# Optimization experiments

Measured on AMD Instinct MI355X. Metric: run time of the kernel, lower is better.

The kernel has to match this reference:

```python
import jax, jax.numpy as jnp
import numpy as np

N_NODES = 20000
N_EDGES = 320000


def gcn_conv(x, W, b, src, dst, n_nodes):
    """PyG GCNConv: add self-loops, symmetric D^-1/2 (A+I) D^-1/2 normalization,
    linear transform then normalized scatter-add aggregation, plus bias."""
    x = x @ W  # [N, out]
    loop = jnp.arange(n_nodes, dtype=src.dtype)
    s = jnp.concatenate([src, loop])  # [E+N]
    d = jnp.concatenate([dst, loop])
    # degree of destination nodes (edge weight = 1), including self-loops
    deg = jax.ops.segment_sum(jnp.ones_like(d, dtype=x.dtype), d, num_segments=n_nodes)
    dinv = jnp.where(deg > 0, jax.lax.rsqrt(deg), 0.0)
    norm = dinv[s] * dinv[d]  # [E+N]
    msg = x[s] * norm[:, None]  # gather + scale, [E+N, out]
    out = jax.ops.segment_sum(msg, d, num_segments=n_nodes)  # scatter-add
    return out + b


def setup_inputs() -> dict:
    key = jax.random.key(0)
    ks = jax.random.split(key, 8)
    x = jax.random.normal(ks[0], (N_NODES, 10), dtype=jnp.float32)
    edge_index = jax.random.randint(ks[1], (2, N_EDGES), 0, N_NODES, dtype=jnp.int32)
    # Glorot-ish init for weights, zero bias (as in PyG defaults)
    def glorot(k, shape):
        lim = float(np.sqrt(6.0 / (shape[0] + shape[1])))
        return jax.random.uniform(k, shape, jnp.float32, -lim, lim)
    return {
        "x": x,
        "edge_index": edge_index,
        "W1": glorot(ks[2], (10, 256)),
        "b1": jnp.zeros((256,), jnp.float32),
        "W2": glorot(ks[3], (256, 128)),
        "b2": jnp.zeros((128,), jnp.float32),
        "W3": glorot(ks[4], (128, 1)),
        "b3": jnp.zeros((1,), jnp.float32),
    }


def reference(x, edge_index, W1, b1, W2, b2, W3, b3):
    src, dst = edge_index[0], edge_index[1]
    n = x.shape[0]
    h = jax.nn.relu(gcn_conv(x, W1, b1, src, dst, n))
    h = jax.nn.relu(gcn_conv(h, W2, b2, src, dst, n))
    out = gcn_conv(h, W3, b3, src, dst, n)
    return out.squeeze(-1)  # [N]
```

## Files before the change

kernel.cpp:

```cpp
#include <hip/hip_runtime.h>
#include <hip/hip_fp16.h>


constexpr int NN  = 20000;
constexpr int NE  = 320000;
constexpr int F0  = 10;
constexpr int F1  = 256;
constexpr int F2  = 128;
constexpr int MB  = 16;
constexpr int CAP = 64;
constexpr int EMAX = 48;

typedef _Float16 f16x8 __attribute__((ext_vector_type(8)));
typedef float    f32x4 __attribute__((ext_vector_type(4)));

constexpr int H1S = 264;
constexpr int BKC = 64;
constexpr int W2S = 72;


__global__ void k_fill(const int* __restrict__ src, const int* __restrict__ dst,
                       int* cursor, int* __restrict__ col) {
  const int t = blockIdx.x * 256 + threadIdx.x;
  if (t * 2 >= NE) return;
  const int2 s2 = *(const int2*)&src[t * 2];
  const int2 d2 = *(const int2*)&dst[t * 2];
  const int p0 = atomicAdd(&cursor[d2.x], 1) & (CAP - 1);
  col[d2.x * CAP + p0] = s2.x;
  const int p1 = atomicAdd(&cursor[d2.y], 1) & (CAP - 1);
  col[d2.y * CAP + p1] = s2.y;
}


__global__ __launch_bounds__(256) void k_prep(const float* __restrict__ W2,
                                              _Float16* __restrict__ W2t,
                                              int* __restrict__ cursor) {
  const int t = blockIdx.x * 256 + threadIdx.x;
  const int n = t >> 8;
  const int k = t & 255;
  W2t[n * 256 + k] = (_Float16)W2[k * F2 + n];
  if (t < NN) cursor[t] = 0;
}


__global__ __launch_bounds__(256) void k_gemm12(
    const float* __restrict__ x, const int* __restrict__ cursor,
    const int* __restrict__ col, const float* __restrict__ W1,
    const float* __restrict__ b1, const _Float16* __restrict__ W2t,
    _Float16* __restrict__ t2h) {
  __shared__ float alds[MB * F0];
  __shared__ float din[MB];
  __shared__ __align__(16) _Float16 h1h[MB * H1S];
  __shared__ __align__(16) _Float16 w2t[F2 * W2S];
  __shared__ unsigned short es[MB][EMAX];
  const int tid = threadIdx.x;
  const int n0 = blockIdx.x * MB;
  const uint4* W2t4 = (const uint4*)W2t;
  const int gb = ((tid >> 3) << 5) + (tid & 7);
  uint4 pf0 = W2t4[gb];
  uint4 pf1 = W2t4[gb + 1024];
  uint4 pf2 = W2t4[gb + 2048];
  uint4 pf3 = W2t4[gb + 3072];
  {
    const int m = tid >> 4;
    const int j0 = tid & 15;
    const int n = n0 + m;
    const int degraw = cursor[n];
    const int deg = min(degraw, EMAX);
    const int base = n * CAP;
    if (j0 == 0) din[m] = rsqrtf((float)(degraw + 1));
    for (int j = j0; j < deg; j += 16)
      es[m][j] = (unsigned short)col[base + j];
  }
  __syncthreads();
  {
    const int m = tid >> 4;
    const int f = tid & 15;
    if (f < F0) {
      const int n = n0 + m;
      const int deg = min(cursor[n], EMAX);
      const float di = din[m];
      float acc = x[n * F0 + f] * di;
      int j = 0;
      for (; j + 3 < deg; j += 4) {
        const int s0 = es[m][j],     s1 = es[m][j + 1];
        const int s2 = es[m][j + 2], s3 = es[m][j + 3];
        const float q0 = rsqrtf((float)(cursor[s0] + 1));
        const float q1 = rsqrtf((float)(cursor[s1] + 1));
        const float q2 = rsqrtf((float)(cursor[s2] + 1));
        const float q3 = rsqrtf((float)(cursor[s3] + 1));
        acc += x[s0 * F0 + f] * q0 + x[s1 * F0 + f] * q1 +
               x[s2 * F0 + f] * q2 + x[s3 * F0 + f] * q3;
      }
      for (; j < deg; ++j) {
        const int s = es[m][j];
        acc += x[s * F0 + f] * rsqrtf((float)(cursor[s] + 1));
      }
      alds[m * F0 + f] = di * acc;
    }
  }
  __syncthreads();
  {
    const int c = tid;
    float w1r[F0];
#pragma unroll
    for (int k = 0; k < F0; ++k) w1r[k] = W1[k * F1 + c];
    const float bb = b1[c];
#pragma unroll
    for (int m = 0; m < MB; ++m) {
      float acc = bb;
#pragma unroll
      for (int k = 0; k < F0; ++k) acc += alds[m * F0 + k] * w1r[k];
      h1h[m * H1S + c] = (_Float16)fmaxf(acc, 0.f);
    }
  }
  const int lane = tid & 63;
  const int wv   = tid >> 6;
  const int lr   = lane & 15;
  const int lg   = lane >> 4;
  const int nt0  = wv * 32;
  f32x4 acc0 = {0.f, 0.f, 0.f, 0.f};
  f32x4 acc1 = {0.f, 0.f, 0.f, 0.f};
  uint4* w2t4 = (uint4*)w2t;
  const int sb = (tid >> 3) * 9 + (tid & 7);
  for (int kc = 0; kc < F1 / BKC; ++kc) {
    __syncthreads();
    w2t4[sb]       = pf0;
    w2t4[sb + 288] = pf1;
    w2t4[sb + 576] = pf2;
    w2t4[sb + 864] = pf3;
    __syncthreads();
    if (kc + 1 < F1 / BKC) {
      const uint4* gnext = W2t4 + (kc + 1) * 8;
      pf0 = gnext[gb];
      pf1 = gnext[gb + 1024];
      pf2 = gnext[gb + 2048];
      pf3 = gnext[gb + 3072];
    }
#pragma unroll
    for (int ks = 0; ks < 2; ++ks) {
      const int kb = kc * BKC + ks * 32;
      const f16x8 av = *(const f16x8*)&h1h[lr * H1S + kb + lg * 8];
      const f16x8 b0 = *(const f16x8*)&w2t[(nt0 + lr) * W2S + ks * 32 + lg * 8];
      const f16x8 b1v = *(const f16x8*)&w2t[(nt0 + 16 + lr) * W2S + ks * 32 + lg * 8];
      acc0 = __builtin_amdgcn_mfma_f32_16x16x32_f16(av, b0, acc0, 0, 0, 0);
      acc1 = __builtin_amdgcn_mfma_f32_16x16x32_f16(av, b1v, acc1, 0, 0, 0);
    }
  }
#pragma unroll
  for (int r = 0; r < 4; ++r) {
    const int row = lg * 4 + r;
    const float dn = din[row];
    t2h[(size_t)(n0 + row) * F2 + nt0 + lr]      = (_Float16)(acc0[r] * dn);
    t2h[(size_t)(n0 + row) * F2 + nt0 + 16 + lr] = (_Float16)(acc1[r] * dn);
  }
}


__device__ inline void acc_h4(uint2 u, float& a0, float& a1, float& a2, float& a3) {
  union { uint2 u; __half2 h[2]; } pk;
  pk.u = u;
  const float2 f0 = __half22float2(pk.h[0]);
  const float2 f1 = __half22float2(pk.h[1]);
  a0 += f0.x; a1 += f0.y; a2 += f1.x; a3 += f1.y;
}

__global__ __launch_bounds__(256) void k_agg2(
    const __half* __restrict__ t2h, const int* __restrict__ cursor,
    const int* __restrict__ col, const float* __restrict__ b2,
    const float* __restrict__ W3, float* __restrict__ t3s) {
  const int wave = (blockIdx.x * 256 + threadIdx.x) >> 6;
  const int lane = threadIdx.x & 63;
  const int half = lane >> 5;
  const int li   = lane & 31;
  const int n    = wave * 2 + half;
  if (n >= NN) return;
  const int deg = cursor[n];
  const int base = n * CAP;
  const int fx = li * 4;
  float a0 = 0.f, a1 = 0.f, a2 = 0.f, a3 = 0.f;
  acc_h4(*(const uint2*)&t2h[(size_t)n * F2 + fx], a0, a1, a2, a3);
  int k = 0;
  for (; k + 15 < deg; k += 16) {
    int ss[16];
#pragma unroll
    for (int j = 0; j < 16; ++j) ss[j] = col[base + k + j];
    uint2 vv[16];
#pragma unroll
    for (int j = 0; j < 16; ++j)
      vv[j] = *(const uint2*)&t2h[(size_t)ss[j] * F2 + fx];
#pragma unroll
    for (int j = 0; j < 16; ++j) acc_h4(vv[j], a0, a1, a2, a3);
  }
  for (; k + 7 < deg; k += 8) {
    int ss[8];
#pragma unroll
    for (int j = 0; j < 8; ++j) ss[j] = col[base + k + j];
    uint2 vv[8];
#pragma unroll
    for (int j = 0; j < 8; ++j)
      vv[j] = *(const uint2*)&t2h[(size_t)ss[j] * F2 + fx];
#pragma unroll
    for (int j = 0; j < 8; ++j) acc_h4(vv[j], a0, a1, a2, a3);
  }
  for (; k + 3 < deg; k += 4) {
    int ss[4];
#pragma unroll
    for (int j = 0; j < 4; ++j) ss[j] = col[base + k + j];
    uint2 vv[4];
#pragma unroll
    for (int j = 0; j < 4; ++j)
      vv[j] = *(const uint2*)&t2h[(size_t)ss[j] * F2 + fx];
#pragma unroll
    for (int j = 0; j < 4; ++j) acc_h4(vv[j], a0, a1, a2, a3);
  }
  for (; k < deg; ++k) {
    acc_h4(*(const uint2*)&t2h[(size_t)col[base + k] * F2 + fx], a0, a1, a2, a3);
  }
  const float di = rsqrtf((float)(deg + 1));
  const float4 bb = *(const float4*)&b2[fx];
  const float4 w3 = *(const float4*)&W3[fx];
  const float h0 = fmaxf(di * a0 + bb.x, 0.f);
  const float h1 = fmaxf(di * a1 + bb.y, 0.f);
  const float h2 = fmaxf(di * a2 + bb.z, 0.f);
  const float h3 = fmaxf(di * a3 + bb.w, 0.f);
  float p = (h0 * w3.x + h1 * w3.y) + (h2 * w3.z + h3 * w3.w);
#pragma unroll
  for (int off = 16; off > 0; off >>= 1) p += __shfl_down(p, off);
  if (li == 0) t3s[n] = di * p;
}


__global__ __launch_bounds__(256) void k_agg3(
    const float* __restrict__ t3s, const int* __restrict__ cursor,
    const int* __restrict__ col, const float* __restrict__ b3,
    float* __restrict__ out) {
  const int wave = (blockIdx.x * 256 + threadIdx.x) >> 6;
  const int lane = threadIdx.x & 63;
  const int sub  = lane >> 4;
  const int li   = lane & 15;
  const int n    = wave * 4 + sub;
  if (n >= NN) return;
  const int deg = cursor[n];
  const int base = n * CAP;
  float acc = 0.f;
  for (int j = li; j < deg; j += 16) acc += t3s[col[base + j]];
  acc += __shfl_xor(acc, 8);
  acc += __shfl_xor(acc, 4);
  acc += __shfl_xor(acc, 2);
  acc += __shfl_xor(acc, 1);
  if (li == 0)
    out[n] = rsqrtf((float)(deg + 1)) * (acc + t3s[n]) + b3[0];
}

extern "C" void kernel_launch(void* const* d_in, const int* in_sizes, int n_in,
                              void* d_out, int out_size, void* d_ws, size_t ws_size,
                              hipStream_t stream) {
  const float* x = (const float*)d_in[0];
  const int* ei = (const int*)d_in[1];
  const int* srcv = ei;
  const int* dstv = ei + NE;
  const float* W1 = (const float*)d_in[2];
  const float* b1 = (const float*)d_in[3];
  const float* W2 = (const float*)d_in[4];
  const float* b2 = (const float*)d_in[5];
  const float* W3 = (const float*)d_in[6];
  const float* b3 = (const float*)d_in[7];
  float* out = (float*)d_out;

  char* w = (char*)d_ws;
  auto alloc = [&](size_t bytes) -> void* {
    void* p = (void*)w;
    w += (bytes + 255) & ~(size_t)255;
    return p;
  };
  int*      cursor = (int*)     alloc(NN * 4);
  int*      col    = (int*)     alloc((size_t)NN * CAP * 4);
  _Float16* t2h    = (_Float16*)alloc((size_t)NN * F2 * 2);
  float*    t3s    = (float*)   alloc(NN * 4);
  _Float16* W2t    = (_Float16*)alloc((size_t)F2 * F1 * 2);

  k_prep<<<(F1 * F2) / 256, 256, 0, stream>>>(W2, W2t, cursor);
  k_fill<<<(NE / 2 + 255) / 256, 256, 0, stream>>>(srcv, dstv, cursor, col);
  k_gemm12<<<NN / MB, 256, 0, stream>>>(x, cursor, col, W1, b1, W2t, t2h);
  k_agg2<<<NN / 8, 256, 0, stream>>>((const __half*)t2h, cursor, col, b2, W3, t3s);
  k_agg3<<<(NN + 15) / 16, 256, 0, stream>>>(t3s, cursor, col, b3, out);
}
```

Before: 122.7 us.

## Pre-swizzle W2 into MFMA fragment order and load B directly from global

```diff
diff --git a/kernel.cpp b/kernel.cpp
--- a/kernel.cpp
+++ b/kernel.cpp
@@ -15,8 +15,6 @@
 typedef float    f32x4 __attribute__((ext_vector_type(4)));
 
 constexpr int H1S = 264;
-constexpr int BKC = 64;
-constexpr int W2S = 72;
 
 
 __global__ void k_fill(const int* __restrict__ src, const int* __restrict__ dst,
@@ -36,9 +34,13 @@
                                               _Float16* __restrict__ W2t,
                                               int* __restrict__ cursor) {
   const int t = blockIdx.x * 256 + threadIdx.x;
-  const int n = t >> 8;
-  const int k = t & 255;
-  W2t[n * 256 + k] = (_Float16)W2[k * F2 + n];
+  const int i    = t & 7;
+  const int lane = (t >> 3) & 63;
+  const int ks   = (t >> 9) & 7;
+  const int tile = t >> 12;
+  const int n = tile * 16 + (lane & 15);
+  const int k = ks * 32 + (lane >> 4) * 8 + i;
+  W2t[t] = (_Float16)W2[k * F2 + n];
   if (t < NN) cursor[t] = 0;
 }
 
@@ -51,16 +53,9 @@
   __shared__ float alds[MB * F0];
   __shared__ float din[MB];
   __shared__ __align__(16) _Float16 h1h[MB * H1S];
-  __shared__ __align__(16) _Float16 w2t[F2 * W2S];
   __shared__ unsigned short es[MB][EMAX];
   const int tid = threadIdx.x;
   const int n0 = blockIdx.x * MB;
-  const uint4* W2t4 = (const uint4*)W2t;
-  const int gb = ((tid >> 3) << 5) + (tid & 7);
-  uint4 pf0 = W2t4[gb];
-  uint4 pf1 = W2t4[gb + 1024];
-  uint4 pf2 = W2t4[gb + 2048];
-  uint4 pf3 = W2t4[gb + 3072];
   {
     const int m = tid >> 4;
     const int j0 = tid & 15;
@@ -114,6 +109,7 @@
       h1h[m * H1S + c] = (_Float16)fmaxf(acc, 0.f);
     }
   }
+  __syncthreads();
   const int lane = tid & 63;
   const int wv   = tid >> 6;
   const int lr   = lane & 15;
@@ -121,31 +117,15 @@
   const int nt0  = wv * 32;
   f32x4 acc0 = {0.f, 0.f, 0.f, 0.f};
   f32x4 acc1 = {0.f, 0.f, 0.f, 0.f};
-  uint4* w2t4 = (uint4*)w2t;
-  const int sb = (tid >> 3) * 9 + (tid & 7);
-  for (int kc = 0; kc < F1 / BKC; ++kc) {
-    __syncthreads();
-    w2t4[sb]       = pf0;
-    w2t4[sb + 288] = pf1;
-    w2t4[sb + 576] = pf2;
-    w2t4[sb + 864] = pf3;
-    __syncthreads();
-    if (kc + 1 < F1 / BKC) {
-      const uint4* gnext = W2t4 + (kc + 1) * 8;
-      pf0 = gnext[gb];
-      pf1 = gnext[gb + 1024];
-      pf2 = gnext[gb + 2048];
-      pf3 = gnext[gb + 3072];
-    }
-#pragma unroll
-    for (int ks = 0; ks < 2; ++ks) {
-      const int kb = kc * BKC + ks * 32;
-      const f16x8 av = *(const f16x8*)&h1h[lr * H1S + kb + lg * 8];
-      const f16x8 b0 = *(const f16x8*)&w2t[(nt0 + lr) * W2S + ks * 32 + lg * 8];
-      const f16x8 b1v = *(const f16x8*)&w2t[(nt0 + 16 + lr) * W2S + ks * 32 + lg * 8];
-      acc0 = __builtin_amdgcn_mfma_f32_16x16x32_f16(av, b0, acc0, 0, 0, 0);
-      acc1 = __builtin_amdgcn_mfma_f32_16x16x32_f16(av, b1v, acc1, 0, 0, 0);
-    }
+  const f16x8* bfrag = (const f16x8*)W2t;
+  const int t0 = wv * 2, t1 = t0 + 1;
+#pragma unroll
+  for (int ks = 0; ks < 8; ++ks) {
+    const f16x8 av  = *(const f16x8*)&h1h[lr * H1S + ks * 32 + lg * 8];
+    const f16x8 b0  = bfrag[(t0 * 8 + ks) * 64 + lane];
+    const f16x8 b1v = bfrag[(t1 * 8 + ks) * 64 + lane];
+    acc0 = __builtin_amdgcn_mfma_f32_16x16x32_f16(av, b0, acc0, 0, 0, 0);
+    acc1 = __builtin_amdgcn_mfma_f32_16x16x32_f16(av, b1v, acc1, 0, 0, 0);
   }
 #pragma unroll
   for (int r = 0; r < 4; ++r) {
```

Measured after the change: 120.9 us. About the same (-1.5%).
